# Kernel tuning notes

Hardware: AMD Instinct MI355X
Metric: run time of the kernel (lower is better)

## Reference

```python
import jax, jax.numpy as jnp
import numpy as np

DT = 0.02        # time step
DT_SKIP = DT * 20
ITERS = 49       # BDF2 iterations hardcoded in forward()
P = 64           # tronc (reduced dim)
NG_U = 8000      # HR sample count, u-equation
NG_V = 8000      # HR sample count, v-equation
B = 32           # batch of trajectories


def setup_inputs() -> dict:
    key = jax.random.key(0)
    k0, k1, k2, k3, k4 = jax.random.split(key, 5)
    state = jax.random.normal(k0, (B, P), dtype=jnp.float32)
    Ap = jax.random.normal(k1, (P, P), dtype=jnp.float32) * 0.05
    W_all_u = jax.random.normal(k2, (4 * NG_U, P), dtype=jnp.float32) * 0.02
    W_all_v = jax.random.normal(k3, (4 * NG_V, P), dtype=jnp.float32) * 0.02
    P_proj = jax.random.normal(k4, (P, NG_U + NG_V), dtype=jnp.float32) * 0.02
    return {"state": state, "Ap": Ap, "W_all_u": W_all_u,
            "W_all_v": W_all_v, "P_proj": P_proj}


def _rhs(a, W_all_u, W_all_v, P_proj):
    # a: (B, p) -> (B, p). Batched hyper-reduced quadratic RHS.
    zu = a @ W_all_u.T                       # (B, 4*Ng_u)
    uu, vu, dxu, dyu = jnp.split(zu, 4, axis=1)
    fu = uu * dxu + vu * dyu                 # (B, Ng_u)
    zv = a @ W_all_v.T                       # (B, 4*Ng_v)
    uv, vv, dxv, dyv = jnp.split(zv, 4, axis=1)
    fv = uv * dxv + vv * dyv                 # (B, Ng_v)
    concat = jnp.concatenate([fu, fv], axis=1)  # (B, Ng_u+Ng_v)
    return -(concat @ P_proj.T)              # (B, p)


def reference(state, Ap, W_all_u, W_all_v, P_proj):
    dt = jnp.float32(DT)
    a0 = state[:, :P]                        # state_rom (B, p)
    eye = jnp.eye(P, dtype=state.dtype)
    mat_1st = eye - dt * Ap[:P, :P]          # I - dt*A
    mat_2nd = 3.0 * eye - 2.0 * dt * Ap[:P, :P]

    # first step: implicit Euler
    f0 = _rhs(a0, W_all_u, W_all_v, P_proj)
    r0 = a0 + dt * f0
    a1 = jnp.linalg.solve(mat_1st, r0.T).T   # == lu_solve(LU_1st, ...)

    # BDF2 recurrence
    def step(carry, _):
        a_prev, f_prev, a_new = carry
        f_new = _rhs(a_new, W_all_u, W_all_v, P_proj)
        r = 4.0 * a_new - a_prev + 4.0 * dt * f_new - 2.0 * dt * f_prev
        a_next = jnp.linalg.solve(mat_2nd, r.T).T
        return (a_new, f_new, a_next), None

    (_, _, out_new), _ = jax.lax.scan(step, (a0, f0, a1), None, length=ITERS)
    return (out_new - a0) / jnp.float32(DT_SKIP)
```

## Files before the change

### kernel.cpp

```cpp
#include <hip/hip_runtime.h>

#define DTC 0.02f
#define INV_DT_SKIP 2.5f
#define NBLK 32
#define NSTEP 50

typedef __attribute__((ext_vector_type(8))) __bf16 bf16x8;
typedef __attribute__((ext_vector_type(4))) float f32x4;
typedef __attribute__((ext_vector_type(8))) unsigned short us8;
typedef unsigned long long u64t;

__device__ inline unsigned short f2bf(float x) {
    unsigned u = __float_as_uint(x);
    unsigned r = u + 0x7FFF + ((u >> 16) & 1u);
    return (unsigned short)(r >> 16);
}
__device__ inline float bf2f(unsigned short h) {
    return __uint_as_float(((unsigned)h) << 16);
}
__device__ inline unsigned pack2(float a, float b) {
    return (unsigned)f2bf(a) | ((unsigned)f2bf(b) << 16);
}
__device__ inline void gstore32(unsigned* p, unsigned v) {
    __hip_atomic_store(p, v, __ATOMIC_RELAXED, __HIP_MEMORY_SCOPE_AGENT);
}
__device__ inline unsigned gload32(const unsigned* p) {
    return __hip_atomic_load(p, __ATOMIC_RELAXED, __HIP_MEMORY_SCOPE_AGENT);
}
__device__ inline u64t gload64(const u64t* p) {
    return __hip_atomic_load(p, __ATOMIC_RELAXED, __HIP_MEMORY_SCOPE_AGENT);
}
#define PINV(x) asm volatile("" : "+v"(x))

__global__ __launch_bounds__(256) void kinv(const float* __restrict__ Ap,
                                            float* __restrict__ inv1,
                                            float* __restrict__ inv2) {
    const int t = threadIdx.x;
    const float coef  = (blockIdx.x == 0) ? DTC : (2.0f * DTC / 3.0f);
    const float scale = (blockIdx.x == 0) ? 1.0f : (1.0f / 3.0f);
    float* outp = (blockIdx.x == 0) ? inv1 : inv2;

    __shared__ float ET[64 * 68];
    __shared__ float XA[64 * 68];
    __shared__ float XB[64 * 68];

    for (int idx = t; idx < 4096; idx += 256) {
        int r = idx >> 6, c = idx & 63;
        float e = coef * Ap[idx];
        ET[c * 68 + r] = e;
        XA[r * 68 + c] = ((r == c) ? 1.0f : 0.0f) + e;
    }
    __syncthreads();

    const int rr = (t >> 4) << 2;
    const int cc = (t & 15) << 2;
    float* bufs[2] = {XA, XB};
    for (int it = 0; it < 3; it++) {
        const float* Xin = bufs[it & 1];
        float* Xout = bufs[(it + 1) & 1];
        float acc[4][4];
        #pragma unroll
        for (int i = 0; i < 4; i++)
            #pragma unroll
            for (int j = 0; j < 4; j++)
                acc[i][j] = ((rr + i) == (cc + j)) ? 1.0f : 0.0f;
        for (int k = 0; k < 64; k++) {
            float4 e4 = *(const float4*)&ET[k * 68 + rr];
            float4 x4 = *(const float4*)&Xin[k * 68 + cc];
            float ev[4] = {e4.x, e4.y, e4.z, e4.w};
            float xv[4] = {x4.x, x4.y, x4.z, x4.w};
            #pragma unroll
            for (int i = 0; i < 4; i++)
                #pragma unroll
                for (int j = 0; j < 4; j++)
                    acc[i][j] += ev[i] * xv[j];
        }
        __syncthreads();
        #pragma unroll
        for (int i = 0; i < 4; i++)
            #pragma unroll
            for (int j = 0; j < 4; j++)
                Xout[(rr + i) * 68 + cc + j] = acc[i][j];
        __syncthreads();
    }
    const float* Xf = bufs[1];
    for (int idx = t; idx < 4096; idx += 256) {
        int r = idx >> 6, c = idx & 63;
        outp[idx] = scale * Xf[r * 68 + c];
    }
}

__global__ void kzero(unsigned* __restrict__ flags) {
    if (threadIdx.x < NBLK) flags[threadIdx.x] = 0u;
}

__global__ __launch_bounds__(512, 2)
void kmain(const float* __restrict__ state,
           const float* __restrict__ Wu,
           const float* __restrict__ Wv,
           const float* __restrict__ Pp,
           const float* __restrict__ inv1,
           const float* __restrict__ inv2,
           unsigned* __restrict__ pbuf,
           unsigned* __restrict__ flags,
           float* __restrict__ out) {
    const int t = threadIdx.x;
    const int l = t & 63;
    const int w = t >> 6;
    const int blk = blockIdx.x;
    const int gw = blk * 8 + w;
    const bool active = (gw < 250);

    __shared__ float Ab[3][2176];
    __shared__ float fb[8][16][36];
    __shared__ float red2[2][8][1024];
    __shared__ float rbuf[32 * 68];

    for (int i = t; i < 2048; i += 512) Ab[0][(i >> 6) * 68 + (i & 63)] = state[i];
    if (!active) {
        for (int i = l; i < 1024; i += 64) { red2[0][w][i] = 0.f; red2[1][w][i] = 0.f; }
    }

    const int nr = l & 15;
    const int c0 = (l >> 4) << 3;
    const int cA = gw * 2;
    const float* W = (cA < 250) ? Wu : Wv;
    const int glA = ((cA < 250) ? cA : cA - 250) * 32;

    bf16x8 wf[2][2][4][2], pf[2][4], sfw[2];
    if (active) {
        #pragma unroll
        for (int ch = 0; ch < 2; ch++)
            #pragma unroll
            for (int th = 0; th < 2; th++)
                #pragma unroll
                for (int rb = 0; rb < 4; rb++)
                    #pragma unroll
                    for (int kt = 0; kt < 2; kt++) {
                        const float* s = W + (size_t)(rb * 8000 + glA + ch * 32 + th * 16 + nr) * 64
                                           + kt * 32 + c0;
                        us8 o;
                        #pragma unroll
                        for (int j = 0; j < 8; j++) o[j] = f2bf(s[j]);
                        wf[ch][th][rb][kt] = __builtin_bit_cast(bf16x8, o);
                    }
        #pragma unroll
        for (int ch = 0; ch < 2; ch++)
            #pragma unroll
            for (int pt = 0; pt < 4; pt++) {
                const float* s = Pp + (size_t)(pt * 16 + nr) * 16000 + (cA + ch) * 32 + c0;
                us8 o;
                #pragma unroll
                for (int j = 0; j < 8; j++) o[j] = f2bf(s[j]);
                pf[ch][pt] = __builtin_bit_cast(bf16x8, o);
            }
    }
    {
        const int ptS = w & 3;
        #pragma unroll
        for (int kt = 0; kt < 2; kt++) {
            int p = ptS * 16 + nr;
            const float* s = inv2 + (size_t)p * 64 + kt * 32 + c0;
            us8 o;
            #pragma unroll
            for (int j = 0; j < 8; j++) {
                float v = s[j] - ((p == kt * 32 + c0 + j) ? (1.0f / 3.0f) : 0.0f);
                o[j] = f2bf(v);
            }
            sfw[kt] = __builtin_bit_cast(bf16x8, o);
        }
    }
    #pragma unroll
    for (int ch = 0; ch < 2; ch++) {
        #pragma unroll
        for (int th = 0; th < 2; th++)
            #pragma unroll
            for (int rb = 0; rb < 4; rb++)
                #pragma unroll
                for (int kt = 0; kt < 2; kt++) PINV(wf[ch][th][rb][kt]);
        #pragma unroll
        for (int pt = 0; pt < 4; pt++) PINV(pf[ch][pt]);
    }
    PINV(sfw[0]); PINV(sfw[1]);
    __syncthreads();

    int ia_prev = 2, ia_cur = 0, ia_next = 1;
    float fprev[4];

    for (int k = 0; k < NSTEP; k++) {
        const int par = k & 1;
        unsigned* pslot = pbuf + (size_t)par * (NBLK * 1024) + blk * 1024;

        if (active) {
            const int col = l & 15, q4 = l >> 4;
            #pragma unroll
            for (int mt = 0; mt < 2; mt++) {
                bf16x8 ahi[2], alo[2];
                {
                    const float* ac = Ab[ia_cur];
                    #pragma unroll
                    for (int kt = 0; kt < 2; kt++) {
                        us8 hv, lv;
                        #pragma unroll
                        for (int j = 0; j < 8; j++) {
                            float x = ac[(mt * 16 + nr) * 68 + kt * 32 + c0 + j];
                            unsigned short h = f2bf(x);
                            hv[j] = h;
                            lv[j] = f2bf(x - bf2f(h));
                        }
                        ahi[kt] = __builtin_bit_cast(bf16x8, hv);
                        alo[kt] = __builtin_bit_cast(bf16x8, lv);
                    }
                }
                f32x4 racc[4] = {{0.f,0.f,0.f,0.f},{0.f,0.f,0.f,0.f},
                                 {0.f,0.f,0.f,0.f},{0.f,0.f,0.f,0.f}};
                #pragma unroll
                for (int ch = 0; ch < 2; ch++) {
                    #pragma unroll
                    for (int th = 0; th < 2; th++) {
                        f32x4 z[4];
                        #pragma unroll
                        for (int rb = 0; rb < 4; rb++) {
                            f32x4 acc = {0.f, 0.f, 0.f, 0.f};
                            #pragma unroll
                            for (int kt = 0; kt < 2; kt++) {
                                acc = __builtin_amdgcn_mfma_f32_16x16x32_bf16(ahi[kt], wf[ch][th][rb][kt], acc, 0, 0, 0);
                                acc = __builtin_amdgcn_mfma_f32_16x16x32_bf16(alo[kt], wf[ch][th][rb][kt], acc, 0, 0, 0);
                            }
                            z[rb] = acc;
                        }
                        #pragma unroll
                        for (int r = 0; r < 4; r++) {
                            float f = z[0][r] * z[2][r] + z[1][r] * z[3][r];
                            fb[w][q4 * 4 + r][th * 16 + col] = f;
                        }
                    }
                    bf16x8 ff;
                    {
                        us8 fv8;
                        #pragma unroll
                        for (int j = 0; j < 8; j++) fv8[j] = f2bf(fb[w][nr][c0 + j]);
                        ff = __builtin_bit_cast(bf16x8, fv8);
                    }
                    #pragma unroll
                    for (int pt = 0; pt < 4; pt++)
                        racc[pt] = __builtin_amdgcn_mfma_f32_16x16x32_bf16(ff, pf[ch][pt], racc[pt], 0, 0, 0);
                }
                #pragma unroll
                for (int pt = 0; pt < 4; pt++)
                    #pragma unroll
                    for (int r = 0; r < 4; r++)
                        red2[mt][w][(q4 * 4 + r) * 64 + pt * 16 + col] = racc[pt][r];
            }
        }
        __syncthreads();

        #pragma unroll
        for (int mt = 0; mt < 2; mt++) {
            float s0 = 0.f, s1 = 0.f;
            #pragma unroll
            for (int w8 = 0; w8 < 8; w8++) {
                s0 += red2[mt][w8][2 * t];
                s1 += red2[mt][w8][2 * t + 1];
            }
            gstore32(&pslot[mt * 512 + t], pack2(s0, s1));
        }
        __syncthreads();

        if (t == 0) gstore32(&flags[blk], (unsigned)(k + 1));
        {
            const unsigned target = (unsigned)(k + 1);
            for (;;) {
                unsigned v = gload32(&flags[l & (NBLK - 1)]);
                if (__all(v >= target)) break;
                __builtin_amdgcn_s_sleep(1);
            }
            asm volatile("" ::: "memory");
        }

        float fv[4];
        {
            const u64t* pb = (const u64t*)(pbuf + (size_t)par * (NBLK * 1024));
            float s0 = 0.f, s1 = 0.f, s2 = 0.f, s3 = 0.f;
            #pragma unroll
            for (int s = 0; s < NBLK; s++) {
                u64t v = gload64(pb + (size_t)s * 512 + t);
                unsigned lo = (unsigned)v, hi = (unsigned)(v >> 32);
                s0 += __uint_as_float(lo << 16);
                s1 += __uint_as_float(lo & 0xffff0000u);
                s2 += __uint_as_float(hi << 16);
                s3 += __uint_as_float(hi & 0xffff0000u);
            }
            fv[0] = -s0; fv[1] = -s1; fv[2] = -s2; fv[3] = -s3;
        }

        {
            const int b = (4 * t) >> 6, p0 = (4 * t) & 63;
            #pragma unroll
            for (int jj = 0; jj < 4; jj++) {
                float f = fv[jj];
                int row = b * 68 + p0 + jj;
                float av = Ab[ia_cur][row];
                float rv = (k == 0) ? (av + DTC * f)
                                    : (4.f * av - Ab[ia_prev][row]
                                       + 4.f * DTC * f - 2.f * DTC * fprev[jj]);
                rbuf[row] = rv;
                fprev[jj] = f;
            }
        }
        __syncthreads();

        {
            const int mtS = w >> 2, ptS = w & 3;
            const int col = l & 15, q4 = l >> 4;
            bf16x8 S0, S1;
            float cb;
            if (k == 0) {
                #pragma unroll
                for (int kt = 0; kt < 2; kt++) {
                    int p = ptS * 16 + nr;
                    const float* s = inv1 + (size_t)p * 64 + kt * 32 + c0;
                    us8 o;
                    #pragma unroll
                    for (int j = 0; j < 8; j++) {
                        float v = s[j] - ((p == kt * 32 + c0 + j) ? 1.0f : 0.0f);
                        o[j] = f2bf(v);
                    }
                    if (kt == 0) S0 = __builtin_bit_cast(bf16x8, o);
                    else         S1 = __builtin_bit_cast(bf16x8, o);
                }
                cb = 1.0f;
            } else {
                S0 = sfw[0]; S1 = sfw[1];
                cb = 1.0f / 3.0f;
            }
            bf16x8 rhi[2], rlo[2];
            #pragma unroll
            for (int kt = 0; kt < 2; kt++) {
                us8 hv, lv;
                #pragma unroll
                for (int j = 0; j < 8; j++) {
                    float x = rbuf[(mtS * 16 + nr) * 68 + kt * 32 + c0 + j];
                    unsigned short h = f2bf(x);
                    hv[j] = h;
                    lv[j] = f2bf(x - bf2f(h));
                }
                rhi[kt] = __builtin_bit_cast(bf16x8, hv);
                rlo[kt] = __builtin_bit_cast(bf16x8, lv);
            }
            f32x4 acc;
            #pragma unroll
            for (int r = 0; r < 4; r++)
                acc[r] = rbuf[(mtS * 16 + q4 * 4 + r) * 68 + ptS * 16 + col] * cb;
            acc = __builtin_amdgcn_mfma_f32_16x16x32_bf16(rhi[0], S0, acc, 0, 0, 0);
            acc = __builtin_amdgcn_mfma_f32_16x16x32_bf16(rlo[0], S0, acc, 0, 0, 0);
            acc = __builtin_amdgcn_mfma_f32_16x16x32_bf16(rhi[1], S1, acc, 0, 0, 0);
            acc = __builtin_amdgcn_mfma_f32_16x16x32_bf16(rlo[1], S1, acc, 0, 0, 0);
            #pragma unroll
            for (int r = 0; r < 4; r++)
                Ab[ia_next][(mtS * 16 + q4 * 4 + r) * 68 + ptS * 16 + col] = acc[r];
        }
        __syncthreads();

        if (k == NSTEP - 1 && blk == 0) {
            for (int i = t; i < 2048; i += 512)
                out[i] = (Ab[ia_next][(i >> 6) * 68 + (i & 63)] - state[i]) * INV_DT_SKIP;
        }

        int tmp = ia_prev; ia_prev = ia_cur; ia_cur = ia_next; ia_next = tmp;
    }
}

extern "C" void kernel_launch(void* const* d_in, const int* in_sizes, int n_in,
                              void* d_out, int out_size, void* d_ws, size_t ws_size,
                              hipStream_t stream) {
    const float* state = (const float*)d_in[0];
    const float* Ap    = (const float*)d_in[1];
    const float* Wu    = (const float*)d_in[2];
    const float* Wv    = (const float*)d_in[3];
    const float* Pp    = (const float*)d_in[4];
    float* out = (float*)d_out;
    float* ws  = (float*)d_ws;

    float* inv1 = ws;
    float* inv2 = ws + 4096;
    unsigned* flags = (unsigned*)(ws + 8192);
    unsigned* pbuf  = (unsigned*)(ws + 8192 + 64);

    hipLaunchKernelGGL(kzero, dim3(1), dim3(64), 0, stream, flags);
    hipLaunchKernelGGL(kinv, dim3(2), dim3(256), 0, stream, Ap, inv1, inv2);
    hipLaunchKernelGGL(kmain, dim3(NBLK), dim3(512), 0, stream,
                       state, Wu, Wv, Pp, inv1, inv2, pbuf, flags, out);
}
```

Baseline: 551.3 us.

## Replace flag barrier with tagged partial sums polled directly across blocks

Removes the per-step grid flag barrier. Each block now writes its fp32 partial sums with a 4-bit step tag in the low mantissa bits, and consumers poll the partial buffer until every slot carries the current tag. Partial sums move from bf16-packed to tag-stamped fp32, and the loads are issued in software-pipelined groups. The zeroing kernel is folded into the inverse kernel, which now clears the larger buffer. This removes one barrier round trip and a __syncthreads per step. In exchange it drops 4 mantissa bits and relies on per-64-bit atomic visibility for correctness.

```diff
diff --git a/kernel.cpp b/kernel.cpp
--- a/kernel.cpp
+++ b/kernel.cpp
@@ -18,14 +18,8 @@
 __device__ inline float bf2f(unsigned short h) {
     return __uint_as_float(((unsigned)h) << 16);
 }
-__device__ inline unsigned pack2(float a, float b) {
-    return (unsigned)f2bf(a) | ((unsigned)f2bf(b) << 16);
-}
-__device__ inline void gstore32(unsigned* p, unsigned v) {
+__device__ inline void gstore64(u64t* p, u64t v) {
     __hip_atomic_store(p, v, __ATOMIC_RELAXED, __HIP_MEMORY_SCOPE_AGENT);
-}
-__device__ inline unsigned gload32(const unsigned* p) {
-    return __hip_atomic_load(p, __ATOMIC_RELAXED, __HIP_MEMORY_SCOPE_AGENT);
 }
 __device__ inline u64t gload64(const u64t* p) {
     return __hip_atomic_load(p, __ATOMIC_RELAXED, __HIP_MEMORY_SCOPE_AGENT);
@@ -34,8 +28,13 @@
 
 __global__ __launch_bounds__(256) void kinv(const float* __restrict__ Ap,
                                             float* __restrict__ inv1,
-                                            float* __restrict__ inv2) {
+                                            float* __restrict__ inv2,
+                                            uint4* __restrict__ pz) {
     const int t = threadIdx.x;
+    {
+        const int gt = blockIdx.x * 256 + t;
+        for (int i = gt; i < 32768; i += 512) pz[i] = (uint4){0u, 0u, 0u, 0u};
+    }
     const float coef  = (blockIdx.x == 0) ? DTC : (2.0f * DTC / 3.0f);
     const float scale = (blockIdx.x == 0) ? 1.0f : (1.0f / 3.0f);
     float* outp = (blockIdx.x == 0) ? inv1 : inv2;
@@ -88,10 +87,6 @@
         int r = idx >> 6, c = idx & 63;
         outp[idx] = scale * Xf[r * 68 + c];
     }
-}
-
-__global__ void kzero(unsigned* __restrict__ flags) {
-    if (threadIdx.x < NBLK) flags[threadIdx.x] = 0u;
 }
 
 __global__ __launch_bounds__(512, 2)
@@ -102,7 +97,6 @@
            const float* __restrict__ inv1,
            const float* __restrict__ inv2,
            unsigned* __restrict__ pbuf,
-           unsigned* __restrict__ flags,
            float* __restrict__ out) {
     const int t = threadIdx.x;
     const int l = t & 63;
@@ -189,7 +183,8 @@
 
     for (int k = 0; k < NSTEP; k++) {
         const int par = k & 1;
-        unsigned* pslot = pbuf + (size_t)par * (NBLK * 1024) + blk * 1024;
+        const unsigned tag = (unsigned)(k + 1) & 15u;
+        unsigned* pslot = pbuf + (size_t)par * (NBLK * 2048) + blk * 2048;
 
         if (active) {
             const int col = l & 15, q4 = l >> 4;
@@ -255,56 +250,109 @@
         }
         __syncthreads();
 
-        #pragma unroll
-        for (int mt = 0; mt < 2; mt++) {
-            float s0 = 0.f, s1 = 0.f;
-            #pragma unroll
-            for (int w8 = 0; w8 < 8; w8++) {
-                s0 += red2[mt][w8][2 * t];
-                s1 += red2[mt][w8][2 * t + 1];
-            }
-            gstore32(&pslot[mt * 512 + t], pack2(s0, s1));
-        }
-        __syncthreads();
-
-        if (t == 0) gstore32(&flags[blk], (unsigned)(k + 1));
         {
-            const unsigned target = (unsigned)(k + 1);
-            for (;;) {
-                unsigned v = gload32(&flags[l & (NBLK - 1)]);
-                if (__all(v >= target)) break;
-                __builtin_amdgcn_s_sleep(1);
-            }
-            asm volatile("" ::: "memory");
+            u64t* ps64 = (u64t*)pslot;
+            #pragma unroll
+            for (int mt = 0; mt < 2; mt++) {
+                float s0 = 0.f, s1 = 0.f;
+                #pragma unroll
+                for (int w8 = 0; w8 < 8; w8++) {
+                    s0 += red2[mt][w8][2 * t];
+                    s1 += red2[mt][w8][2 * t + 1];
+                }
+                unsigned u0 = (__float_as_uint(s0) & ~15u) | tag;
+                unsigned u1 = (__float_as_uint(s1) & ~15u) | tag;
+                gstore64(&ps64[mt * 512 + t], (u64t)u0 | ((u64t)u1 << 32));
+            }
+        }
+
+        float rb_[4];
+        const int bB = (4 * t) >> 6, p0B = (4 * t) & 63;
+        {
+            #pragma unroll
+            for (int jj = 0; jj < 4; jj++) {
+                int row = bB * 68 + p0B + jj;
+                float av = Ab[ia_cur][row];
+                rb_[jj] = (k == 0) ? av
+                                   : (4.f * av - Ab[ia_prev][row] - 2.f * DTC * fprev[jj]);
+            }
         }
 
         float fv[4];
         {
-            const u64t* pb = (const u64t*)(pbuf + (size_t)par * (NBLK * 1024));
+            const u64t* pb = (const u64t*)(pbuf + (size_t)par * (NBLK * 2048));
             float s0 = 0.f, s1 = 0.f, s2 = 0.f, s3 = 0.f;
-            #pragma unroll
-            for (int s = 0; s < NBLK; s++) {
-                u64t v = gload64(pb + (size_t)s * 512 + t);
-                unsigned lo = (unsigned)v, hi = (unsigned)(v >> 32);
-                s0 += __uint_as_float(lo << 16);
-                s1 += __uint_as_float(lo & 0xffff0000u);
-                s2 += __uint_as_float(hi << 16);
-                s3 += __uint_as_float(hi & 0xffff0000u);
-            }
+            unsigned need = 0xFFFFFFFFu;
+
+            u64t b0[8], b1[8], b2[8];
+
+            #define GISSUE(g, B)                                               \
+                _Pragma("unroll")                                              \
+                for (int si = 0; si < 4; si++) {                               \
+                    const u64t* p = pb + (size_t)((g) * 4 + si) * 1024 + 2 * t;\
+                    B[2 * si]     = gload64(p);                                \
+                    B[2 * si + 1] = gload64(p + 1);                            \
+                }
+            #define GVALID(g, B)                                               \
+                _Pragma("unroll")                                              \
+                for (int si = 0; si < 4; si++) {                               \
+                    unsigned a0 = (unsigned)B[2 * si];                         \
+                    unsigned a1 = (unsigned)(B[2 * si] >> 32);                 \
+                    unsigned d0 = (unsigned)B[2 * si + 1];                     \
+                    unsigned d1 = (unsigned)(B[2 * si + 1] >> 32);             \
+                    unsigned bad = ((a0 ^ tag) | (a1 ^ tag) |                  \
+                                    (d0 ^ tag) | (d1 ^ tag)) & 15u;            \
+                    if (bad == 0u) {                                           \
+                        s0 += __uint_as_float(a0 & ~15u);                      \
+                        s1 += __uint_as_float(a1 & ~15u);                      \
+                        s2 += __uint_as_float(d0 & ~15u);                      \
+                        s3 += __uint_as_float(d1 & ~15u);                      \
+                        need &= ~(1u << ((g) * 4 + si));                       \
+                    }                                                          \
+                }
+
+            GISSUE(0, b0); GISSUE(1, b1); GISSUE(2, b2);
+            GVALID(0, b0); GISSUE(3, b0);
+            GVALID(1, b1); GISSUE(4, b1);
+            GVALID(2, b2); GISSUE(5, b2);
+            GVALID(3, b0); GISSUE(6, b0);
+            GVALID(4, b1); GISSUE(7, b1);
+            GVALID(5, b2);
+            GVALID(6, b0);
+            GVALID(7, b1);
+
+            while (need) {
+                #pragma unroll
+                for (int sl = 0; sl < 32; sl++) {
+                    if (need & (1u << sl)) {
+                        const u64t* p = pb + (size_t)sl * 1024 + 2 * t;
+                        u64t v0 = gload64(p), v1 = gload64(p + 1);
+                        unsigned a0 = (unsigned)v0, a1 = (unsigned)(v0 >> 32);
+                        unsigned d0 = (unsigned)v1, d1 = (unsigned)(v1 >> 32);
+                        unsigned bad = ((a0 ^ tag) | (a1 ^ tag) |
+                                        (d0 ^ tag) | (d1 ^ tag)) & 15u;
+                        if (bad == 0u) {
+                            s0 += __uint_as_float(a0 & ~15u);
+                            s1 += __uint_as_float(a1 & ~15u);
+                            s2 += __uint_as_float(d0 & ~15u);
+                            s3 += __uint_as_float(d1 & ~15u);
+                            need &= ~(1u << sl);
+                        }
+                    }
+                }
+            }
+            #undef GISSUE
+            #undef GVALID
+            asm volatile("" ::: "memory");
             fv[0] = -s0; fv[1] = -s1; fv[2] = -s2; fv[3] = -s3;
         }
 
         {
-            const int b = (4 * t) >> 6, p0 = (4 * t) & 63;
+            const float cf = (k == 0) ? DTC : 4.f * DTC;
             #pragma unroll
             for (int jj = 0; jj < 4; jj++) {
                 float f = fv[jj];
-                int row = b * 68 + p0 + jj;
-                float av = Ab[ia_cur][row];
-                float rv = (k == 0) ? (av + DTC * f)
-                                    : (4.f * av - Ab[ia_prev][row]
-                                       + 4.f * DTC * f - 2.f * DTC * fprev[jj]);
-                rbuf[row] = rv;
+                rbuf[bB * 68 + p0B + jj] = rb_[jj] + cf * f;
                 fprev[jj] = f;
             }
         }
@@ -384,11 +432,10 @@
 
     float* inv1 = ws;
     float* inv2 = ws + 4096;
-    unsigned* flags = (unsigned*)(ws + 8192);
-    unsigned* pbuf  = (unsigned*)(ws + 8192 + 64);
-
-    hipLaunchKernelGGL(kzero, dim3(1), dim3(64), 0, stream, flags);
-    hipLaunchKernelGGL(kinv, dim3(2), dim3(256), 0, stream, Ap, inv1, inv2);
+    unsigned* pbuf = (unsigned*)(ws + 8192);
+
+    hipLaunchKernelGGL(kinv, dim3(2), dim3(256), 0, stream, Ap, inv1, inv2,
+                       (uint4*)pbuf);
     hipLaunchKernelGGL(kmain, dim3(NBLK), dim3(512), 0, stream,
-                       state, Wu, Wv, Pp, inv1, inv2, pbuf, flags, out);
-}
+                       state, Wu, Wv, Pp, inv1, inv2, pbuf, out);
+}
```

New measurement: 700.6 us. 27.1% more time.

## Replace block barrier with per-wave atomic arrival and padded reduction buffer

Applied to the files above, without the earlier changes.

Drops the __syncthreads after the cross-wave reduction. Each wave now bumps its block's flag with an atomic add once its own stores have drained, and only wave 0 polls the global flags while the other waves spin on a shared-memory go word. The non-f part of the BDF2 right-hand side is computed before the wait, so it overlaps with the grid-wide barrier. It also pads the red2 reduction rows (1024 to 1056 floats, q4 stride 264) to reduce LDS bank conflicts and reads them as float2. In exchange, the go-word handshake and the relaxed atomics make the memory-ordering and correctness reasoning more delicate.

```diff
diff --git a/kernel.cpp b/kernel.cpp
--- a/kernel.cpp
+++ b/kernel.cpp
@@ -113,12 +113,14 @@
 
     __shared__ float Ab[3][2176];
     __shared__ float fb[8][16][36];
-    __shared__ float red2[2][8][1024];
+    __shared__ float red2[2][8][1056];
     __shared__ float rbuf[32 * 68];
+    __shared__ unsigned go;
 
     for (int i = t; i < 2048; i += 512) Ab[0][(i >> 6) * 68 + (i & 63)] = state[i];
+    if (t == 0) go = 0u;
     if (!active) {
-        for (int i = l; i < 1024; i += 64) { red2[0][w][i] = 0.f; red2[1][w][i] = 0.f; }
+        for (int i = l; i < 1056; i += 64) { red2[0][w][i] = 0.f; red2[1][w][i] = 0.f; }
     }
 
     const int nr = l & 15;
@@ -250,30 +252,58 @@
                 for (int pt = 0; pt < 4; pt++)
                     #pragma unroll
                     for (int r = 0; r < 4; r++)
-                        red2[mt][w][(q4 * 4 + r) * 64 + pt * 16 + col] = racc[pt][r];
+                        red2[mt][w][q4 * 264 + r * 64 + pt * 16 + col] = racc[pt][r];
             }
         }
         __syncthreads();
 
-        #pragma unroll
-        for (int mt = 0; mt < 2; mt++) {
-            float s0 = 0.f, s1 = 0.f;
-            #pragma unroll
-            for (int w8 = 0; w8 < 8; w8++) {
-                s0 += red2[mt][w8][2 * t];
-                s1 += red2[mt][w8][2 * t + 1];
-            }
-            gstore32(&pslot[mt * 512 + t], pack2(s0, s1));
-        }
-        __syncthreads();
-
-        if (t == 0) gstore32(&flags[blk], (unsigned)(k + 1));
-        {
-            const unsigned target = (unsigned)(k + 1);
-            for (;;) {
-                unsigned v = gload32(&flags[l & (NBLK - 1)]);
-                if (__all(v >= target)) break;
-                __builtin_amdgcn_s_sleep(1);
+        {
+            const int q4e = t >> 7;
+            const int rem = (2 * t) & 255;
+            const int addr = q4e * 264 + rem;
+            #pragma unroll
+            for (int mt = 0; mt < 2; mt++) {
+                float s0 = 0.f, s1 = 0.f;
+                #pragma unroll
+                for (int w8 = 0; w8 < 8; w8++) {
+                    float2 p = *(const float2*)&red2[mt][w8][addr];
+                    s0 += p.x;
+                    s1 += p.y;
+                }
+                gstore32(&pslot[mt * 512 + t], pack2(s0, s1));
+            }
+        }
+
+        asm volatile("s_waitcnt vmcnt(0)" ::: "memory");
+        if (l == 0)
+            __hip_atomic_fetch_add(&flags[blk], 1u, __ATOMIC_RELAXED,
+                                   __HIP_MEMORY_SCOPE_AGENT);
+
+        float rb_[4];
+        const int bB = (4 * t) >> 6, p0B = (4 * t) & 63;
+        {
+            #pragma unroll
+            for (int jj = 0; jj < 4; jj++) {
+                int row = bB * 68 + p0B + jj;
+                float av = Ab[ia_cur][row];
+                rb_[jj] = (k == 0) ? av
+                                   : (4.f * av - Ab[ia_prev][row] - 2.f * DTC * fprev[jj]);
+            }
+        }
+
+        {
+            const unsigned target = 8u * (unsigned)(k + 1);
+            if (w == 0) {
+                for (;;) {
+                    unsigned v = gload32(&flags[l & (NBLK - 1)]);
+                    if (__all(v >= target)) break;
+                    __builtin_amdgcn_s_sleep(1);
+                }
+                asm volatile("" ::: "memory");
+                if (l == 0) *(volatile unsigned*)&go = (unsigned)(k + 1);
+            } else {
+                while (*(volatile unsigned*)&go < (unsigned)(k + 1))
+                    __builtin_amdgcn_s_sleep(1);
             }
             asm volatile("" ::: "memory");
         }
@@ -295,16 +325,11 @@
         }
 
         {
-            const int b = (4 * t) >> 6, p0 = (4 * t) & 63;
+            const float cf = (k == 0) ? DTC : 4.f * DTC;
             #pragma unroll
             for (int jj = 0; jj < 4; jj++) {
                 float f = fv[jj];
-                int row = b * 68 + p0 + jj;
-                float av = Ab[ia_cur][row];
-                float rv = (k == 0) ? (av + DTC * f)
-                                    : (4.f * av - Ab[ia_prev][row]
-                                       + 4.f * DTC * f - 2.f * DTC * fprev[jj]);
-                rbuf[row] = rv;
+                rbuf[bB * 68 + p0B + jj] = rb_[jj] + cf * f;
                 fprev[jj] = f;
             }
         }
```

Result: slower. 810.9 us (+47.1%).
